# Performance work log

Measured on AMD Instinct MI355X. Metric: run time of the kernel, lower is better.

## Reference

```python
import jax, jax.numpy as jnp
import numpy as np

IGNORE_INDEX = -100
BETA = 0.1
B, T, H, V = 4, 512, 4096, 32000

def setup_inputs() -> dict:
    key = jax.random.key(0)
    ks = jax.random.split(key, 8)
    s = 1.0 / np.sqrt(H)
    return {
        "_input": jax.random.normal(ks[0], (B, T, H), jnp.float32),
        "weight": jax.random.normal(ks[1], (V, H), jnp.float32) * s,
        "bias": jax.random.normal(ks[2], (V,), jnp.float32) * 0.01,
        "target": jax.random.randint(ks[3], (B, T), 0, V, jnp.int64),
        "preference_labels": jax.random.bernoulli(ks[4], 0.5, (B,)),
        "ref_input": jax.random.normal(ks[5], (B, T, H), jnp.float32),
        "ref_weight": jax.random.normal(ks[6], (V, H), jnp.float32) * s,
        "ref_bias": jax.random.normal(ks[7], (V,), jnp.float32) * 0.01,
        "kl": jax.random.uniform(jax.random.fold_in(key, 9), (1,), jnp.float32),
    }

def _avg_log_prob(x, w, b, target):
    # logits: [B, T, V]
    logits = jnp.einsum("bth,vh->btv", x, w) + b
    lse = jax.nn.logsumexp(logits, axis=-1)            # [B, T]
    idx = jnp.clip(target, 0, None)[..., None]
    tgt_logit = jnp.take_along_axis(logits, idx, axis=-1)[..., 0]
    per_tok_logp = tgt_logit - lse                     # [B, T]
    mask = (target != IGNORE_INDEX).astype(per_tok_logp.dtype)
    denom = jnp.maximum(mask.sum(-1), 1.0)
    return (per_tok_logp * mask).sum(-1) / denom       # [B]

def reference(_input, weight, bias, target, preference_labels, ref_input, ref_weight, ref_bias, kl):
    avg_logp = _avg_log_prob(_input, weight, bias, target)
    ref_avg_logp = jax.lax.stop_gradient(_avg_log_prob(ref_input, ref_weight, ref_bias, target))
    logratios = avg_logp - ref_avg_logp                # [B]
    multiplier = jnp.where(preference_labels, 1.0, -1.0)
    losses = 1.0 - jax.nn.sigmoid(BETA * (logratios - kl[0]) * multiplier)
    return losses.sum() / target.shape[0]
```

## Files before the change

kernel.cpp:

```cpp
#include <hip/hip_runtime.h>
#include <hip/hip_bf16.h>
#include <stdint.h>

#define HD 4096
#define VD 32000
#define BT 2048
#define TT 512
#define IGNORE_IDX (-100)

#define BM 256
#define BN 256
#define BKT 64
#define KT (HD / BKT)
#define NB (VD / BN)
#define MB (BT / BM)
#define NWG2 (MB * NB * 2)

#define NCHUNK (VD / 64)

typedef __attribute__((ext_vector_type(8))) short short8;
typedef __attribute__((ext_vector_type(4))) float f32x4;

__device__ __forceinline__ uint16_t f2bf(float f) {
    uint32_t u = __float_as_uint(f);
    u += 0x7FFFu + ((u >> 16) & 1u);
    return (uint16_t)(u >> 16);
}

__device__ __forceinline__ void gload16(const void* g, void* l) {
    __builtin_amdgcn_global_load_lds(
        (const __attribute__((address_space(1))) void*)g,
        (__attribute__((address_space(3))) void*)l, 16, 0, 0);
}

#define SBAR __builtin_amdgcn_sched_barrier(0)

__global__ void convert_x(const float* __restrict__ x0, const float* __restrict__ x1,
                          uint16_t* __restrict__ xbf) {
    const int64_t n4 = (int64_t)BT * HD / 4;
    ushort4* o0 = (ushort4*)xbf;
    ushort4* o1 = (ushort4*)(xbf + (int64_t)BT * HD);
    for (int64_t i = blockIdx.x * (int64_t)blockDim.x + threadIdx.x; i < n4;
         i += (int64_t)gridDim.x * blockDim.x) {
        float4 a = ((const float4*)x0)[i];
        float4 b = ((const float4*)x1)[i];
        ushort4 ua, ub;
        ua.x = f2bf(a.x); ua.y = f2bf(a.y); ua.z = f2bf(a.z); ua.w = f2bf(a.w);
        ub.x = f2bf(b.x); ub.y = f2bf(b.y); ub.z = f2bf(b.z); ub.w = f2bf(b.w);
        o0[i] = ua;
        o1[i] = ub;
    }
}

__global__ void convert_w(const float* __restrict__ w0, const float* __restrict__ w1,
                          uint16_t* __restrict__ wbf) {
    const int64_t n4 = (int64_t)VD * HD / 4;
    ushort4* o0 = (ushort4*)wbf;
    ushort4* o1 = (ushort4*)(wbf + (int64_t)VD * HD);
    for (int64_t i = blockIdx.x * (int64_t)blockDim.x + threadIdx.x; i < n4;
         i += (int64_t)gridDim.x * blockDim.x) {
        float4 a = ((const float4*)w0)[i];
        float4 b = ((const float4*)w1)[i];
        ushort4 ua, ub;
        ua.x = f2bf(a.x); ua.y = f2bf(a.y); ua.z = f2bf(a.z); ua.w = f2bf(a.w);
        ub.x = f2bf(b.x); ub.y = f2bf(b.y); ub.z = f2bf(b.z); ub.w = f2bf(b.w);
        o0[i] = ua;
        o1[i] = ub;
    }
}

__device__ __forceinline__ void mfma16(
    const short8& a0k0, const short8& a0k1, const short8& a1k0, const short8& a1k1,
    const short8 (&bfr)[4][2], f32x4* acc0, f32x4* acc1)
{
    __builtin_amdgcn_s_setprio(1);
#pragma unroll
    for (int ni = 0; ni < 4; ++ni)
        acc0[ni] = __builtin_amdgcn_mfma_f32_16x16x32_bf16(a0k0, bfr[ni][0], acc0[ni], 0, 0, 0);
#pragma unroll
    for (int ni = 0; ni < 4; ++ni)
        acc1[ni] = __builtin_amdgcn_mfma_f32_16x16x32_bf16(a1k0, bfr[ni][0], acc1[ni], 0, 0, 0);
#pragma unroll
    for (int ni = 0; ni < 4; ++ni)
        acc0[ni] = __builtin_amdgcn_mfma_f32_16x16x32_bf16(a0k1, bfr[ni][1], acc0[ni], 0, 0, 0);
#pragma unroll
    for (int ni = 0; ni < 4; ++ni)
        acc1[ni] = __builtin_amdgcn_mfma_f32_16x16x32_bf16(a1k1, bfr[ni][1], acc1[ni], 0, 0, 0);
    __builtin_amdgcn_s_setprio(0);
}

template<int CUR>
__device__ __forceinline__ void tile_body(
    int t,
    const uint16_t* __restrict__ agp, const uint16_t* __restrict__ bgp,
    char* aLdst, char* bLdst,
    const char* pA0, const char* pA1, const char* pB0, const char* pB1,
    f32x4 (&acc)[8][4])
{
    constexpr int CB  = CUR * 32768;
    constexpr int NXB = (CUR ^ 1) * 32768;
    const bool more = (t + 1) < KT;
    const int ko = (t + 1) * BKT;

    if (more) {
#pragma unroll
        for (int j = 0; j < 4; ++j)
            gload16(bgp + (size_t)(j * 32) * HD + ko, bLdst + NXB + j * 4096);
#pragma unroll
        for (int j = 0; j < 4; ++j)
            gload16(agp + (size_t)(j * 32) * HD + ko, aLdst + NXB + j * 4096);
    }
    SBAR;

    short8 bfr[4][2];
#pragma unroll
    for (int ni = 0; ni < 4; ++ni) {
        bfr[ni][0] = *(const short8*)(pB0 + ni * 2048 + CB);
        bfr[ni][1] = *(const short8*)(pB1 + ni * 2048 + CB);
    }
#pragma unroll
    for (int p = 0; p < 4; ++p) {
        const short8 a0 = *(const short8*)(pA0 + (2 * p) * 2048 + CB);
        const short8 a1 = *(const short8*)(pA1 + (2 * p) * 2048 + CB);
        const short8 a2 = *(const short8*)(pA0 + (2 * p + 1) * 2048 + CB);
        const short8 a3 = *(const short8*)(pA1 + (2 * p + 1) * 2048 + CB);
        mfma16(a0, a1, a2, a3, bfr, acc[2 * p], acc[2 * p + 1]);
    }

    SBAR;
    asm volatile("s_waitcnt vmcnt(0)" ::: "memory");
    SBAR;
    __builtin_amdgcn_s_barrier();
    SBAR;
}

__global__ __launch_bounds__(512, 2) void gemm_lse_bf(
    const uint16_t* __restrict__ xbf, const uint16_t* __restrict__ wbf,
    const float* __restrict__ b0, const float* __restrict__ b1,
    const int* __restrict__ target,
    float* __restrict__ partials, float* __restrict__ tgtlog)
{
    __shared__ uint16_t As[2 * BM * BKT];
    __shared__ uint16_t Bs[2 * BN * BKT];

    const int orig = blockIdx.x;
    const int wgid = (orig & 7) * (NWG2 / 8) + (orig >> 3);
    const int mb    = wgid & 7;
    const int rest  = wgid >> 3;
    const int nb    = rest % NB;
    const int model = rest / NB;

    const uint16_t* xb = xbf + (size_t)model * BT * HD;
    const uint16_t* wb = wbf + (size_t)model * VD * HD;
    const float* bias  = model ? b1 : b0;

    const int row0 = mb * BM;
    const int c0   = nb * BN;

    const int tid    = threadIdx.x;
    const int lane   = tid & 63;
    const int wid    = tid >> 6;
    const int wr     = wid >> 2;
    const int wc     = wid & 3;

    const int lane15 = lane & 15;
    const int kg     = lane >> 4;
    const int swz    = (lane & 7) << 4;

    const int srow8 = lane >> 3;
    const int slot  = (lane & 7) ^ srow8;
    const uint16_t* agp = xb + (size_t)(row0 + wr * 128 + wc * 8 + srow8) * HD + slot * 8;
    const int bq = wr * 2 + (wc & 1);
    const uint16_t* bgp = wb + (size_t)(c0 + (wc >> 1) * 128 + bq * 8 + srow8) * HD + slot * 8;
    char* aLdst = (char*)As + wr * 16384 + wc * 1024;
    char* bLdst = (char*)Bs + (wc >> 1) * 16384 + bq * 1024;

    const int arow_b = wr * 128 + lane15;
    const int brow_b = wc * 64 + lane15;
    const char* pA0 = (const char*)As + ((arow_b * 128 + 0  + kg * 16) ^ swz);
    const char* pA1 = (const char*)As + ((arow_b * 128 + 64 + kg * 16) ^ swz);
    const char* pB0 = (const char*)Bs + ((brow_b * 128 + 0  + kg * 16) ^ swz);
    const char* pB1 = (const char*)Bs + ((brow_b * 128 + 64 + kg * 16) ^ swz);

    f32x4 acc[8][4];
#pragma unroll
    for (int i = 0; i < 8; ++i)
#pragma unroll
        for (int j = 0; j < 4; ++j) acc[i][j] = (f32x4){0.f, 0.f, 0.f, 0.f};

#pragma unroll
    for (int j = 0; j < 4; ++j)
        gload16(bgp + (size_t)(j * 32) * HD, bLdst + j * 4096);
#pragma unroll
    for (int j = 0; j < 4; ++j)
        gload16(agp + (size_t)(j * 32) * HD, aLdst + j * 4096);
    SBAR; asm volatile("s_waitcnt vmcnt(0)" ::: "memory"); SBAR;
    __builtin_amdgcn_s_barrier();
    SBAR;

    for (int t2 = 0; t2 < KT; t2 += 2) {
        tile_body<0>(t2,     agp, bgp, aLdst, bLdst, pA0, pA1, pB0, pB1, acc);
        tile_body<1>(t2 + 1, agp, bgp, aLdst, bLdst, pA0, pA1, pB0, pB1, acc);
    }

    float bv4[4];
#pragma unroll
    for (int ni = 0; ni < 4; ++ni) bv4[ni] = bias[c0 + wc * 64 + ni * 16 + lane15];

#pragma unroll
    for (int mi = 0; mi < 8; ++mi) {
        const int grow_base = row0 + wr * 128 + mi * 16 + kg * 4;
#pragma unroll
        for (int j = 0; j < 4; ++j) {
            const int grow = grow_base + j;
            float v[4];
#pragma unroll
            for (int ni = 0; ni < 4; ++ni) v[ni] = acc[mi][ni][j] + bv4[ni];
            float m = fmaxf(fmaxf(v[0], v[1]), fmaxf(v[2], v[3]));
#pragma unroll
            for (int msk = 1; msk < 16; msk <<= 1)
                m = fmaxf(m, __shfl_xor(m, msk));
            float s = __expf(v[0] - m) + __expf(v[1] - m) +
                      __expf(v[2] - m) + __expf(v[3] - m);
#pragma unroll
            for (int msk = 1; msk < 16; msk <<= 1)
                s += __shfl_xor(s, msk);
            const int tg = target[grow];
#pragma unroll
            for (int ni = 0; ni < 4; ++ni) {
                const int gcol = c0 + wc * 64 + ni * 16 + lane15;
                if (tg == gcol) tgtlog[model * BT + grow] = v[ni];
            }
            if (lane15 == 0) {
                const size_t po = ((size_t)(model * BT + grow) * NCHUNK + nb * 4 + wc) * 2;
                partials[po]     = m;
                partials[po + 1] = s;
            }
        }
    }
}

__global__ __launch_bounds__(256) void gemm_lse_f32(
    const uint16_t* __restrict__ xbf,
    const float* __restrict__ w0, const float* __restrict__ b0,
    const float* __restrict__ w1, const float* __restrict__ b1,
    const int* __restrict__ target,
    float* __restrict__ partials, float* __restrict__ tgtlog)
{
    const int orig = blockIdx.x;
    const int wgid = (orig & 7) * 1000 + (orig >> 3);
    const int mb    = wgid & 7;
    const int rest  = wgid >> 3;
    const int chunk = rest % 500;
    const int model = rest / 500;

    const float* w    = model ? w1 : w0;
    const float* bias = model ? b1 : b0;
    const uint16_t* xb = xbf + (size_t)model * BT * HD;

    const int row0 = mb * 256;
    const int c0   = chunk * 64;

    const int tid  = threadIdx.x;
    const int lane = tid & 63;
    const int wid  = tid >> 6;

    __shared__ uint16_t As_[256 * 64];
    __shared__ uint16_t Bs_[64 * 64];

    f32x4 acc[4][4];
#pragma unroll
    for (int i = 0; i < 4; ++i)
#pragma unroll
        for (int j = 0; j < 4; ++j) acc[i][j] = (f32x4){0.f, 0.f, 0.f, 0.f};

    const int srow8 = lane >> 3;
    const int slot  = (lane & 7) ^ srow8;
    const uint16_t* agsrc = xb + (size_t)(row0 + wid * 64 + srow8) * HD + slot * 8;
    char* aldst = (char*)As_ + wid * 8192;

    const int ss   = tid & 7;
    const int srow = tid >> 3;
    const int swz_w = (srow & 7) << 4;
    const float* bptr = w + (size_t)(c0 + srow) * HD + ss * 8;

    const int lane15 = lane & 15;
    const int kg     = lane >> 4;
    const int swz_r  = (lane & 7) << 4;

    for (int kt = 0; kt < 64; ++kt) {
        const int kofs = kt * 64;
#pragma unroll
        for (int c = 0; c < 8; ++c)
            gload16(agsrc + (size_t)c * 8 * HD + kofs, aldst + c * 1024);
        {
            float4 bv[2][2];
#pragma unroll
            for (int r = 0; r < 2; ++r) {
                const float* p = bptr + (size_t)r * 32 * HD + kofs;
                bv[r][0] = *(const float4*)(p);
                bv[r][1] = *(const float4*)(p + 4);
            }
#pragma unroll
            for (int r = 0; r < 2; ++r) {
                const int row_l = srow + r * 32;
                float fv[8] = {bv[r][0].x, bv[r][0].y, bv[r][0].z, bv[r][0].w,
                               bv[r][1].x, bv[r][1].y, bv[r][1].z, bv[r][1].w};
                uint32_t pk[4];
#pragma unroll
                for (int e = 0; e < 4; ++e)
                    pk[e] = (uint32_t)f2bf(fv[2 * e]) | ((uint32_t)f2bf(fv[2 * e + 1]) << 16);
                const int off = (row_l * 128 + ss * 16) ^ swz_w;
                *(uint4*)((char*)Bs_ + off) = *(uint4*)pk;
            }
        }
        __syncthreads();
#pragma unroll
        for (int ks = 0; ks < 2; ++ks) {
            short8 af[4], bf[4];
#pragma unroll
            for (int mi = 0; mi < 4; ++mi) {
                const int arow = wid * 64 + mi * 16 + lane15;
                const int off = (arow * 128 + ks * 64 + kg * 16) ^ swz_r;
                af[mi] = *(const short8*)((const char*)As_ + off);
            }
#pragma unroll
            for (int ni = 0; ni < 4; ++ni) {
                const int brow = ni * 16 + lane15;
                const int off = (brow * 128 + ks * 64 + kg * 16) ^ swz_r;
                bf[ni] = *(const short8*)((const char*)Bs_ + off);
            }
#pragma unroll
            for (int mi = 0; mi < 4; ++mi)
#pragma unroll
                for (int ni = 0; ni < 4; ++ni)
                    acc[mi][ni] = __builtin_amdgcn_mfma_f32_16x16x32_bf16(
                        af[mi], bf[ni], acc[mi][ni], 0, 0, 0);
        }
        __syncthreads();
    }

    float bv4[4];
#pragma unroll
    for (int ni = 0; ni < 4; ++ni) bv4[ni] = bias[c0 + ni * 16 + lane15];

#pragma unroll
    for (int mi = 0; mi < 4; ++mi) {
        const int grow_base = row0 + wid * 64 + mi * 16 + kg * 4;
#pragma unroll
        for (int j = 0; j < 4; ++j) {
            const int grow = grow_base + j;
            float v[4];
#pragma unroll
            for (int ni = 0; ni < 4; ++ni) v[ni] = acc[mi][ni][j] + bv4[ni];
            float m = fmaxf(fmaxf(v[0], v[1]), fmaxf(v[2], v[3]));
#pragma unroll
            for (int msk = 1; msk < 16; msk <<= 1)
                m = fmaxf(m, __shfl_xor(m, msk));
            float s = __expf(v[0] - m) + __expf(v[1] - m) +
                      __expf(v[2] - m) + __expf(v[3] - m);
#pragma unroll
            for (int msk = 1; msk < 16; msk <<= 1)
                s += __shfl_xor(s, msk);
            const int tg = target[grow];
#pragma unroll
            for (int ni = 0; ni < 4; ++ni) {
                const int gcol = c0 + ni * 16 + lane15;
                if (tg == gcol) tgtlog[model * BT + grow] = v[ni];
            }
            if (lane15 == 0) {
                const size_t po = ((size_t)(model * BT + grow) * NCHUNK + chunk) * 2;
                partials[po]     = m;
                partials[po + 1] = s;
            }
        }
    }
}

__global__ void lse_reduce(const float* __restrict__ partials,
                           const float* __restrict__ tgtlog,
                           float* __restrict__ logp) {
    const int gw = blockIdx.x * (blockDim.x >> 6) + (threadIdx.x >> 6);
    if (gw >= 2 * BT) return;
    const int lane = threadIdx.x & 63;
    const float* p = partials + (size_t)gw * NCHUNK * 2;

    float m = -1e30f;
#pragma unroll
    for (int i = 0; i < 8; ++i) {
        const int c = lane + i * 64;
        if (c < NCHUNK) m = fmaxf(m, p[c * 2]);
    }
#pragma unroll
    for (int msk = 1; msk < 64; msk <<= 1) m = fmaxf(m, __shfl_xor(m, msk));
    float s = 0.f;
#pragma unroll
    for (int i = 0; i < 8; ++i) {
        const int c = lane + i * 64;
        if (c < NCHUNK) s += p[c * 2 + 1] * __expf(p[c * 2] - m);
    }
#pragma unroll
    for (int msk = 1; msk < 64; msk <<= 1) s += __shfl_xor(s, msk);
    if (lane == 0) {
        const float lse = m + __logf(s);
        logp[gw] = tgtlog[gw] - lse;
    }
}

__global__ void final_loss(const float* __restrict__ logp, const int* __restrict__ target,
                           const int* __restrict__ pref, const float* __restrict__ kl,
                           float* __restrict__ out) {
    const int t = threadIdx.x;
    const int lane = t & 63, wv = t >> 6;
    __shared__ float rp[4][8], rr[4][8], rm[4][8];
#pragma unroll
    for (int b = 0; b < 4; ++b) {
        const int idx = b * TT + t;
        const int tg = target[idx];
        const bool mk = (tg != IGNORE_IDX);
        float lp = mk ? logp[idx] : 0.f;
        float lr = mk ? logp[BT + idx] : 0.f;
        float mc = mk ? 1.f : 0.f;
        for (int off = 32; off; off >>= 1) {
            lp += __shfl_down(lp, off);
            lr += __shfl_down(lr, off);
            mc += __shfl_down(mc, off);
        }
        if (lane == 0) { rp[b][wv] = lp; rr[b][wv] = lr; rm[b][wv] = mc; }
    }
    __syncthreads();
    if (t == 0) {
        float loss = 0.f;
        for (int b = 0; b < 4; ++b) {
            float sp = 0.f, sr = 0.f, sm = 0.f;
            for (int i = 0; i < 8; ++i) { sp += rp[b][i]; sr += rr[b][i]; sm += rm[b][i]; }
            const float denom = fmaxf(sm, 1.f);
            const float lrb = (sp - sr) / denom;
            const float mult = pref[b] ? 1.f : -1.f;
            const float z = 0.1f * (lrb - kl[0]) * mult;
            loss += 1.f / (1.f + __expf(z));
        }
        out[0] = loss * 0.25f;
    }
}

extern "C" void kernel_launch(void* const* d_in, const int* in_sizes, int n_in,
                              void* d_out, int out_size, void* d_ws, size_t ws_size,
                              hipStream_t stream) {
    const float* x    = (const float*)d_in[0];
    const float* w0   = (const float*)d_in[1];
    const float* b0   = (const float*)d_in[2];
    const int*   tgt  = (const int*)d_in[3];
    const int*   pref = (const int*)d_in[4];
    const float* xr   = (const float*)d_in[5];
    const float* w1   = (const float*)d_in[6];
    const float* b1   = (const float*)d_in[7];
    const float* kl   = (const float*)d_in[8];
    float* out = (float*)d_out;

    const size_t xbf_b  = (size_t)2 * BT * HD * 2;
    const size_t part_b = (size_t)2 * BT * NCHUNK * 2 * 4;
    const size_t tl_b   = (size_t)2 * BT * 4;
    const size_t wbf_b  = (size_t)2 * VD * HD * 2;

    char* wp = (char*)d_ws;
    uint16_t* xbf     = (uint16_t*)wp;                 wp += xbf_b;
    float*    partials = (float*)wp;                   wp += part_b;
    float*    tgtlog   = (float*)wp;                   wp += tl_b;
    float*    logp     = (float*)wp;                   wp += tl_b;
    uint16_t* wbf      = (uint16_t*)wp;
    const bool use_wbf = ws_size >= (xbf_b + part_b + 2 * tl_b + wbf_b);

    hipLaunchKernelGGL(convert_x, dim3(1024), dim3(256), 0, stream, x, xr, xbf);
    if (use_wbf) {
        hipLaunchKernelGGL(convert_w, dim3(4096), dim3(256), 0, stream, w0, w1, wbf);
        hipLaunchKernelGGL(gemm_lse_bf, dim3(NWG2), dim3(512), 0, stream,
                           xbf, wbf, b0, b1, tgt, partials, tgtlog);
    } else {
        hipLaunchKernelGGL(gemm_lse_f32, dim3(8000), dim3(256), 0, stream,
                           xbf, w0, b0, w1, b1, tgt, partials, tgtlog);
    }
    hipLaunchKernelGGL(lse_reduce, dim3(2 * BT / 4), dim3(256), 0, stream,
                       partials, tgtlog, logp);
    hipLaunchKernelGGL(final_loss, dim3(1), dim3(512), 0, stream, logp, tgt, pref, kl, out);
}
```

Baseline: 1.505 ms.

## Load GEMM B operand directly from global into registers, bypass LDS

The weight (B) tile is no longer staged through shared memory. Each wave now prefetches its own B fragments straight from global memory into registers, one K-tile ahead. The A-fragment LDS reads are also interleaved with the MFMA groups, and the wait changes to vmcnt(8) so it only covers the A async copies. This halves LDS usage and drops the B LDS writes and reads, but the two wave rows now fetch the same B data twice from cache. Global-load latency also has to be hidden by a single tile of MFMA work.

Measured after the change: 1.880 ms. 1.25x slower.

```diff
diff --git a/kernel.cpp b/kernel.cpp
--- a/kernel.cpp
+++ b/kernel.cpp
@@ -92,9 +92,11 @@
 template<int CUR>
 __device__ __forceinline__ void tile_body(
     int t,
-    const uint16_t* __restrict__ agp, const uint16_t* __restrict__ bgp,
-    char* aLdst, char* bLdst,
-    const char* pA0, const char* pA1, const char* pB0, const char* pB1,
+    const uint16_t* __restrict__ agp,
+    const uint16_t* (&bgn)[4],
+    char* aLdst,
+    const char* pA0, const char* pA1,
+    short8 (&bfr)[4][2],
     f32x4 (&acc)[8][4])
 {
     constexpr int CB  = CUR * 32768;
@@ -105,30 +107,48 @@
     if (more) {
 #pragma unroll
         for (int j = 0; j < 4; ++j)
-            gload16(bgp + (size_t)(j * 32) * HD + ko, bLdst + NXB + j * 4096);
-#pragma unroll
-        for (int j = 0; j < 4; ++j)
             gload16(agp + (size_t)(j * 32) * HD + ko, aLdst + NXB + j * 4096);
     }
     SBAR;
 
-    short8 bfr[4][2];
-#pragma unroll
-    for (int ni = 0; ni < 4; ++ni) {
-        bfr[ni][0] = *(const short8*)(pB0 + ni * 2048 + CB);
-        bfr[ni][1] = *(const short8*)(pB1 + ni * 2048 + CB);
-    }
-#pragma unroll
-    for (int p = 0; p < 4; ++p) {
-        const short8 a0 = *(const short8*)(pA0 + (2 * p) * 2048 + CB);
-        const short8 a1 = *(const short8*)(pA1 + (2 * p) * 2048 + CB);
-        const short8 a2 = *(const short8*)(pA0 + (2 * p + 1) * 2048 + CB);
-        const short8 a3 = *(const short8*)(pA1 + (2 * p + 1) * 2048 + CB);
-        mfma16(a0, a1, a2, a3, bfr, acc[2 * p], acc[2 * p + 1]);
-    }
-
-    SBAR;
-    asm volatile("s_waitcnt vmcnt(0)" ::: "memory");
+    short8 aX0 = *(const short8*)(pA0 + 0 * 2048 + CB);
+    short8 aX1 = *(const short8*)(pA1 + 0 * 2048 + CB);
+    short8 aX2 = *(const short8*)(pA0 + 1 * 2048 + CB);
+    short8 aX3 = *(const short8*)(pA1 + 1 * 2048 + CB);
+    short8 aY0 = *(const short8*)(pA0 + 2 * 2048 + CB);
+    short8 aY1 = *(const short8*)(pA1 + 2 * 2048 + CB);
+    short8 aY2 = *(const short8*)(pA0 + 3 * 2048 + CB);
+    short8 aY3 = *(const short8*)(pA1 + 3 * 2048 + CB);
+    SBAR;
+    mfma16(aX0, aX1, aX2, aX3, bfr, acc[0], acc[1]);
+    SBAR;
+    aX0 = *(const short8*)(pA0 + 4 * 2048 + CB);
+    aX1 = *(const short8*)(pA1 + 4 * 2048 + CB);
+    aX2 = *(const short8*)(pA0 + 5 * 2048 + CB);
+    aX3 = *(const short8*)(pA1 + 5 * 2048 + CB);
+    SBAR;
+    mfma16(aY0, aY1, aY2, aY3, bfr, acc[2], acc[3]);
+    SBAR;
+    aY0 = *(const short8*)(pA0 + 6 * 2048 + CB);
+    aY1 = *(const short8*)(pA1 + 6 * 2048 + CB);
+    aY2 = *(const short8*)(pA0 + 7 * 2048 + CB);
+    aY3 = *(const short8*)(pA1 + 7 * 2048 + CB);
+    SBAR;
+    mfma16(aX0, aX1, aX2, aX3, bfr, acc[4], acc[5]);
+    SBAR;
+    mfma16(aY0, aY1, aY2, aY3, bfr, acc[6], acc[7]);
+    SBAR;
+
+    if (more) {
+#pragma unroll
+        for (int ni = 0; ni < 4; ++ni) {
+            bgn[ni] += BKT;
+            bfr[ni][0] = *(const short8*)(bgn[ni]);
+            bfr[ni][1] = *(const short8*)(bgn[ni] + 32);
+        }
+    }
+    SBAR;
+    asm volatile("s_waitcnt vmcnt(8)" ::: "memory");
     SBAR;
     __builtin_amdgcn_s_barrier();
     SBAR;
@@ -141,7 +161,6 @@
     float* __restrict__ partials, float* __restrict__ tgtlog)
 {
     __shared__ uint16_t As[2 * BM * BKT];
-    __shared__ uint16_t Bs[2 * BN * BKT];
 
     const int orig = blockIdx.x;
     const int wgid = (orig & 7) * (NWG2 / 8) + (orig >> 3);
@@ -170,17 +189,16 @@
     const int srow8 = lane >> 3;
     const int slot  = (lane & 7) ^ srow8;
     const uint16_t* agp = xb + (size_t)(row0 + wr * 128 + wc * 8 + srow8) * HD + slot * 8;
-    const int bq = wr * 2 + (wc & 1);
-    const uint16_t* bgp = wb + (size_t)(c0 + (wc >> 1) * 128 + bq * 8 + srow8) * HD + slot * 8;
     char* aLdst = (char*)As + wr * 16384 + wc * 1024;
-    char* bLdst = (char*)Bs + (wc >> 1) * 16384 + bq * 1024;
 
     const int arow_b = wr * 128 + lane15;
-    const int brow_b = wc * 64 + lane15;
     const char* pA0 = (const char*)As + ((arow_b * 128 + 0  + kg * 16) ^ swz);
     const char* pA1 = (const char*)As + ((arow_b * 128 + 64 + kg * 16) ^ swz);
-    const char* pB0 = (const char*)Bs + ((brow_b * 128 + 0  + kg * 16) ^ swz);
-    const char* pB1 = (const char*)Bs + ((brow_b * 128 + 64 + kg * 16) ^ swz);
+
+    const uint16_t* bgn[4];
+#pragma unroll
+    for (int ni = 0; ni < 4; ++ni)
+        bgn[ni] = wb + (size_t)(c0 + wc * 64 + ni * 16 + lane15) * HD + kg * 8;
 
     f32x4 acc[8][4];
 #pragma unroll
@@ -188,19 +206,23 @@
 #pragma unroll
         for (int j = 0; j < 4; ++j) acc[i][j] = (f32x4){0.f, 0.f, 0.f, 0.f};
 
-#pragma unroll
-    for (int j = 0; j < 4; ++j)
-        gload16(bgp + (size_t)(j * 32) * HD, bLdst + j * 4096);
+    short8 bfr[4][2];
+
 #pragma unroll
     for (int j = 0; j < 4; ++j)
         gload16(agp + (size_t)(j * 32) * HD, aLdst + j * 4096);
-    SBAR; asm volatile("s_waitcnt vmcnt(0)" ::: "memory"); SBAR;
+#pragma unroll
+    for (int ni = 0; ni < 4; ++ni) {
+        bfr[ni][0] = *(const short8*)(bgn[ni]);
+        bfr[ni][1] = *(const short8*)(bgn[ni] + 32);
+    }
+    SBAR; asm volatile("s_waitcnt vmcnt(8)" ::: "memory"); SBAR;
     __builtin_amdgcn_s_barrier();
     SBAR;
 
     for (int t2 = 0; t2 < KT; t2 += 2) {
-        tile_body<0>(t2,     agp, bgp, aLdst, bLdst, pA0, pA1, pB0, pB1, acc);
-        tile_body<1>(t2 + 1, agp, bgp, aLdst, bLdst, pA0, pA1, pB0, pB1, acc);
+        tile_body<0>(t2,     agp, bgn, aLdst, pA0, pA1, bfr, acc);
+        tile_body<1>(t2 + 1, agp, bgn, aLdst, pA0, pA1, bfr, acc);
     }
 
     float bv4[4];
```
